# Optimization experiments

Measured on AMD Instinct MI355X. Metric: run time of the kernel, lower is better.

## Reference

```python
import jax, jax.numpy as jnp
import numpy as np

NPOINT, RADIUS, NSAMPLE = 512, 0.2, 32
EPS = 1e-5
CHANNELS = [67, 64, 64, 128]


def _fps(pts, npoint):
    # pts: [B, N, 3]; deterministic start at index 0 (torch impl uses randint)
    B, N, _ = pts.shape
    def body(carry, _):
        mind, far = carry
        c = jnp.take_along_axis(pts, far[:, None, None], axis=1)         # [B,1,3]
        mind = jnp.minimum(mind, jnp.sum((pts - c) ** 2, axis=-1))
        return (mind, jnp.argmax(mind, axis=-1).astype(jnp.int32)), far
    init = (jnp.full((B, N), 1e10, pts.dtype), jnp.zeros((B,), jnp.int32))
    _, idxs = jax.lax.scan(body, init, None, length=npoint)
    return idxs.T                                                         # [B, npoint]


def _gather(p, idx):
    # p: [B, N, C], idx: [B, ...] -> [B, ..., C]
    return jax.vmap(lambda pp, ii: pp[ii])(p, idx)


def _cbr(x, w, b, g, be, m, v):
    # Conv3d kernel [1, 4, 1]; torch padding='same' on even kernel -> (lo=1, hi=2) on t axis
    y = jax.lax.conv_general_dilated(x, w, (1, 1, 1),
                                     [(0, 0), (1, 2), (0, 0)],
                                     dimension_numbers=('NCDHW', 'OIDHW', 'NCDHW'))
    ex = lambda a: a[None, :, None, None, None]
    y = y + ex(b)
    # BatchNorm3d (eval mode with running stats)
    y = (y - ex(m)) * ex(g / jnp.sqrt(v + EPS)) + ex(be)
    return jax.nn.relu(y)


def _forward(xyz, points, params):
    B, t, _, N = xyz.shape
    S, K = NPOINT, NSAMPLE
    xf = jnp.transpose(xyz, (0, 1, 3, 2)).reshape(B * t, N, 3)            # [BT,N,3]
    pf = jnp.transpose(points, (0, 1, 3, 2)).reshape(B * t, N, -1)        # [BT,N,D]
    fidx = _fps(xf.reshape(B, t, N, 3)[:, 0], S)                          # [B,S], FPS on frame 0
    fidx_bt = jnp.broadcast_to(fidx[:, None, :], (B, t, S)).reshape(B * t, S)
    new_xyz = _gather(xf, fidx_bt)                                        # [BT,S,3]
    # squared distances via matmul form (matches square_distance)
    sq = (jnp.sum(new_xyz ** 2, -1)[:, :, None] + jnp.sum(xf ** 2, -1)[:, None, :]
          - 2.0 * jnp.einsum('bsc,bnc->bsn', new_xyz, xf))                # [BT,S,N]
    # ball query: invalid -> N, sort indices, take first K, fallback to first valid
    gidx = jnp.where(sq > RADIUS ** 2, N, jnp.arange(N, dtype=jnp.int32)[None, None, :])
    gidx = jnp.sort(gidx, axis=-1)[:, :, :K]                              # [BT,S,K]
    gidx = jnp.where(gidx == N, gidx[:, :, :1], gidx)
    gxyz = _gather(xf, gidx) - new_xyz[:, :, None, :]                     # [BT,S,K,3]
    feat = jnp.concatenate([gxyz, _gather(pf, gidx)], axis=-1)            # [BT,S,K,3+D]
    feat = feat.reshape(B, t, S, K, -1).transpose(0, 4, 2, 1, 3)          # [B,C,S,t,K]
    for p in params:
        feat = _cbr(feat, *p)
    feat = jnp.max(feat, axis=-1)                                         # [B,C',S,t]
    new_points = jnp.transpose(feat, (0, 3, 1, 2))                        # [B,t,C',S]
    new_xyz = new_xyz.reshape(B, t, S, 3).transpose(0, 1, 3, 2)           # [B,t,3,S]
    return new_xyz, new_points


def setup_inputs() -> dict:
    key = jax.random.key(0)
    ks = jax.random.split(key, 40)
    B, t, D, N = 2, 8, 64, 1024
    inp = {
        'xyz': jax.random.uniform(ks[0], (B, t, 3, N), jnp.float32),
        'points': jax.random.normal(ks[1], (B, t, D, N), jnp.float32),
    }
    j = 2
    for i in range(3):
        ci, co = CHANNELS[i], CHANNELS[i + 1]
        inp[f'w{i}'] = jax.random.normal(ks[j], (co, ci, 1, 4, 1), jnp.float32) * 0.05; j += 1
        inp[f'b{i}'] = jax.random.normal(ks[j], (co,), jnp.float32) * 0.01; j += 1
        inp[f'g{i}'] = jax.random.uniform(ks[j], (co,), jnp.float32, 0.5, 1.5); j += 1
        inp[f'be{i}'] = jax.random.normal(ks[j], (co,), jnp.float32) * 0.1; j += 1
        inp[f'm{i}'] = jax.random.normal(ks[j], (co,), jnp.float32) * 0.1; j += 1
        inp[f'v{i}'] = jax.random.uniform(ks[j], (co,), jnp.float32, 0.5, 1.5); j += 1
    return inp


def reference(xyz, points, w0, b0, g0, be0, m0, v0, w1, b1, g1, be1, m1, v1, w2, b2, g2, be2, m2, v2):
    params = [(w0, b0, g0, be0, m0, v0), (w1, b1, g1, be1, m1, v1), (w2, b2, g2, be2, m2, v2)]
    return _forward(xyz, points, params)
```

## Files before the change

kernel.cpp:

```cpp
#include <hip/hip_runtime.h>
#include <math.h>

#define NPTS 1024
#define S_   512
#define T_   8
#define K_   32
#define B_   2

typedef short bf16x8 __attribute__((ext_vector_type(8)));
typedef short short4v __attribute__((ext_vector_type(4)));
typedef float f32x4 __attribute__((ext_vector_type(4)));
typedef float vf2 __attribute__((ext_vector_type(2)));

static __device__ __forceinline__ short f2bf(float f) {
    unsigned u = __float_as_uint(f);
    unsigned r = (u + 0x7FFFu + ((u >> 16) & 1u)) >> 16;
    return (short)r;
}

template <int CTRL>
static __device__ __forceinline__ float dppmaxf(float x) {
    int mv = __builtin_amdgcn_update_dpp(0, __float_as_int(x), CTRL, 0xF, 0xF, true);
    return fmaxf(x, __int_as_float(mv));
}
static __device__ __forceinline__ unsigned wavemax_bits_f(float x) {
    x = dppmaxf<0x111>(x); x = dppmaxf<0x112>(x);
    x = dppmaxf<0x114>(x); x = dppmaxf<0x118>(x);
    x = dppmaxf<0x142>(x); x = dppmaxf<0x143>(x);
    return (unsigned)__builtin_amdgcn_readlane(__float_as_int(x), 63);
}

static __device__ __forceinline__ vf2 pk_sub(vf2 a, vf2 b) { return a - b; }
static __device__ __forceinline__ vf2 pk_fma(vf2 a, vf2 b, vf2 c) {
#if __has_builtin(__builtin_elementwise_fma)
    return __builtin_elementwise_fma(a, b, c);
#else
    vf2 r; r[0] = __fmaf_rn(a[0], b[0], c[0]); r[1] = __fmaf_rn(a[1], b[1], c[1]); return r;
#endif
}
static __device__ __forceinline__ vf2 pk_min(vf2 a, vf2 b) {
#if __has_builtin(__builtin_elementwise_min)
    return __builtin_elementwise_min(a, b);
#else
    vf2 r; r[0] = fminf(a[0], b[0]); r[1] = fminf(a[1], b[1]); return r;
#endif
}
static __device__ __forceinline__ vf2 pk_max(vf2 a, vf2 b) {
#if __has_builtin(__builtin_elementwise_max)
    return __builtin_elementwise_max(a, b);
#else
    vf2 r; r[0] = fmaxf(a[0], b[0]); r[1] = fmaxf(a[1], b[1]); return r;
#endif
}

__global__ __launch_bounds__(64) void fps_kernel(const float* __restrict__ xyz,
                                                 int* __restrict__ fidx)
{
    int b    = blockIdx.x;
    int lane = threadIdx.x;
    __shared__ float4 sc[NPTS];
    const float* bx = xyz + (size_t)b * (T_ * 3 * NPTS);
    vf2 px2[8], py2[8], pz2[8], mind2[8];
#pragma unroll
    for (int q = 0; q < 4; ++q) {
        float4 vx = ((const float4*)(bx))[lane * 4 + q];
        float4 vy = ((const float4*)(bx + NPTS))[lane * 4 + q];
        float4 vz = ((const float4*)(bx + 2 * NPTS))[lane * 4 + q];
        px2[q*2]   = (vf2){vx.x, vx.y};  px2[q*2+1] = (vf2){vx.z, vx.w};
        py2[q*2]   = (vf2){vy.x, vy.y};  py2[q*2+1] = (vf2){vy.z, vy.w};
        pz2[q*2]   = (vf2){vz.x, vz.y};  pz2[q*2+1] = (vf2){vz.z, vz.w};
        int n0 = lane * 16 + q * 4;
        sc[n0+0] = make_float4(vx.x, vy.x, vz.x, 0.f);
        sc[n0+1] = make_float4(vx.y, vy.y, vz.y, 0.f);
        sc[n0+2] = make_float4(vx.z, vy.z, vz.z, 0.f);
        sc[n0+3] = make_float4(vx.w, vy.w, vz.w, 0.f);
        mind2[q*2] = (vf2){1e10f, 1e10f}; mind2[q*2+1] = (vf2){1e10f, 1e10f};
    }
    __syncthreads();

    int far = 0;
    for (int it = 0; it < S_; ++it) {
        if (lane == 0) fidx[b * S_ + it] = far;
        float4 c = sc[far];
        vf2 c2x = (vf2){c.x, c.x}, c2y = (vf2){c.y, c.y}, c2z = (vf2){c.z, c.z};
#pragma unroll
        for (int q = 0; q < 8; ++q) {
            vf2 dx = pk_sub(px2[q], c2x);
            vf2 dy = pk_sub(py2[q], c2y);
            vf2 dz = pk_sub(pz2[q], c2z);
            vf2 d  = pk_fma(dz, dz, pk_fma(dy, dy, dx * dx));
            mind2[q] = pk_min(mind2[q], d);
        }
        vf2 t4a = pk_max(mind2[0], mind2[4]);
        vf2 t4b = pk_max(mind2[1], mind2[5]);
        vf2 t4c = pk_max(mind2[2], mind2[6]);
        vf2 t4d = pk_max(mind2[3], mind2[7]);
        vf2 t2a = pk_max(t4a, t4c);
        vf2 t2b = pk_max(t4b, t4d);
        vf2 t1  = pk_max(t2a, t2b);
        float lmax = fmaxf(t1[0], t1[1]);
        unsigned maxb = wavemax_bits_f(lmax);
        int cj[16];
#pragma unroll
        for (int j = 0; j < 16; ++j)
            cj[j] = (__float_as_uint(mind2[j >> 1][j & 1]) == maxb) ? j : 64;
        int m8[8], m4[4], m2v[2];
#pragma unroll
        for (int j = 0; j < 8; ++j) m8[j] = min(cj[j], cj[j + 8]);
#pragma unroll
        for (int j = 0; j < 4; ++j) m4[j] = min(m8[j], m8[j + 4]);
        m2v[0] = min(m4[0], m4[2]); m2v[1] = min(m4[1], m4[3]);
        int minj = min(m2v[0], m2v[1]);
        unsigned long long mk = __ballot(minj < 64);
        int l0 = __ffsll((long long)mk) - 1;
        int jw = __builtin_amdgcn_readlane(minj, l0);
        far = l0 * 16 + jw;
    }
}

__global__ __launch_bounds__(256) void transpose_points(
    const float* __restrict__ pts, short* __restrict__ ptsT)
{
    int nt = blockIdx.x;
    int bt = blockIdx.y;
    __shared__ float tile[64][65];
    int tid = threadIdx.x;
    for (int e = tid; e < 4096; e += 256) {
        int ci = e >> 6, nn = e & 63;
        tile[ci][nn] = pts[((size_t)bt * 64 + ci) * NPTS + nt * 64 + nn];
    }
    __syncthreads();
    for (int e = tid; e < 4096; e += 256) {
        int nn = e >> 6, ci = e & 63;
        ptsT[((size_t)bt * NPTS + nt * 64 + nn) * 64 + ci] = f2bf(tile[ci][nn]);
    }
}

template <int CI, int CIp, int CO, bool PERM>
__global__ __launch_bounds__(256) void prep_w(const float* __restrict__ w,
                                              short* __restrict__ wg)
{
    int e = blockIdx.x * 256 + threadIdx.x;
    if (e >= 4 * CO * CIp) return;
    int dt = e / (CO * CIp);
    int rem = e - dt * (CO * CIp);
    int co = rem / CIp;
    int ci = rem - co * CIp;
    float val = 0.0f;
    if (PERM) {
        int cref = (ci < 64) ? (ci + 3) : ((ci < 67) ? (ci - 64) : -1);
        if (cref >= 0) val = w[((size_t)co * CI + cref) * 4 + dt];
    } else {
        if (ci < CI) val = w[((size_t)co * CI + ci) * 4 + dt];
    }
    wg[e] = f2bf(val);
}

__global__ void ballquery_kernel(const float* __restrict__ xyz,
                                 const int* __restrict__ fidx,
                                 int* __restrict__ gidx,
                                 float* __restrict__ newxyz,
                                 float* __restrict__ out0)
{
    int s    = blockIdx.x;
    int bt   = blockIdx.y;
    int b    = bt >> 3;
    int lane = threadIdx.x;
    const float* bx = xyz + (size_t)bt * 3 * NPTS;
    int fid = fidx[b * S_ + s];
    float nx = bx[fid], ny = bx[NPTS + fid], nz = bx[2 * NPTS + fid];
    if (lane < 3) {
        float vv = (lane == 0) ? nx : ((lane == 1) ? ny : nz);
        out0[(bt * 3 + lane) * S_ + s]   = vv;
        newxyz[(bt * S_ + s) * 3 + lane] = vv;
    }
    float A = __fmaf_rn(nz, nz, __fmaf_rn(ny, ny, __fmul_rn(nx, nx)));
    const float R2 = (float)(0.2 * 0.2);
    int* g = gidx + (size_t)(bt * S_ + s) * K_;
    int count = 0, firstIdx = -1;
    for (int j = 0; j < 16; ++j) {
        if (count >= K_) break;
        int n = j * 64 + lane;
        float x = bx[n], y = bx[NPTS + n], z = bx[2 * NPTS + n];
        float Bn = __fmaf_rn(z, z, __fmaf_rn(y, y, __fmul_rn(x, x)));
        float C  = __fmaf_rn(nz, z, __fmaf_rn(ny, y, __fmul_rn(nx, x)));
        float sq = __fsub_rn(__fadd_rn(A, Bn), __fmul_rn(2.0f, C));
        bool valid = !(sq > R2);
        unsigned long long mb = __ballot(valid);
        if (valid) {
            int pos = count + __popcll(mb & ((1ull << lane) - 1ull));
            if (pos < K_) g[pos] = n;
        }
        if (firstIdx < 0 && mb) firstIdx = j * 64 + (__ffsll((long long)mb) - 1);
        count += __popcll(mb);
    }
    if (count < K_) {
        for (int p = count + lane; p < K_; p += 64) g[p] = firstIdx;
    }
}

template <int CI, int CIp, int NK, int CO, bool GATHER, bool POOL>
__global__ __launch_bounds__(256) void conv_mfma(
    const short* __restrict__ actIn,
    const float* __restrict__ xyz, const short* __restrict__ ptsT,
    const int* __restrict__ gidx, const float* __restrict__ newxyz,
    const short* __restrict__ wg, const float* __restrict__ bb,
    const float* __restrict__ gg, const float* __restrict__ be,
    const float* __restrict__ mm, const float* __restrict__ vv,
    short* __restrict__ actOut, float* __restrict__ outPool)
{
    __shared__ __align__(16) short xs[256 * CIp];
    int s = blockIdx.x, b = blockIdx.y;
    int co_base = blockIdx.z * 64;
    int tid = threadIdx.x;

    {
        int col = tid;
        short* xrow = &xs[col * CIp];
        if (GATHER) {
            int k = col & 31, tt = col >> 5;
            int bt = b * T_ + tt;
            int idx = gidx[((size_t)bt * S_ + s) * K_ + k];
            const short* prow = ptsT + ((size_t)bt * NPTS + idx) * 64;
#pragma unroll
            for (int c = 0; c < 8; ++c)
                ((int4*)xrow)[c] = ((const int4*)prow)[c];
            const float* nxp = &newxyz[((size_t)bt * S_ + s) * 3];
#pragma unroll
            for (int ci = 0; ci < 3; ++ci)
                xrow[64 + ci] = f2bf(xyz[(size_t)(bt * 3 + ci) * NPTS + idx] - nxp[ci]);
            for (int ci = 67; ci < CIp; ++ci) xrow[ci] = 0;
        } else {
            const short* src = actIn + (((size_t)b * S_ + s) * 256 + col) * 64;
#pragma unroll
            for (int c = 0; c < 8; ++c)
                ((int4*)xrow)[c] = ((const int4*)src)[c];
            for (int ci = 64; ci < CIp; ++ci) xrow[ci] = 0;
        }
    }
    __syncthreads();

    int lane = tid & 63;
    int wv   = tid >> 6;
    int l16  = lane & 15;
    int lq   = lane >> 4;

    f32x4 acc[16];
#pragma unroll
    for (int nb = 0; nb < 16; ++nb) acc[nb] = (f32x4){0.f, 0.f, 0.f, 0.f};

#pragma unroll
    for (int ks = 0; ks < NK; ++ks) {
        bf16x8 afr[4];
#pragma unroll
        for (int dt = 0; dt < 4; ++dt)
            afr[dt] = *(const bf16x8*)&wg[((size_t)(dt * CO + co_base + wv * 16 + l16)) * CIp + ks * 32 + lq * 8];
        bf16x8 bfr[16];
#pragma unroll
        for (int cb = 0; cb < 16; ++cb)
            bfr[cb] = *(const bf16x8*)&xs[(cb * 16 + l16) * CIp + ks * 32 + lq * 8];
#pragma unroll
        for (int dt = 0; dt < 4; ++dt) {
#pragma unroll
            for (int nb = 0; nb < 16; ++nb) {
                int cb = nb + (dt - 1) * 2;
                if (cb >= 0 && cb < 16)
                    acc[nb] = __builtin_amdgcn_mfma_f32_16x16x32_bf16(
                        afr[dt], bfr[cb], acc[nb], 0, 0, 0);
            }
        }
    }

    float sc[4], c2[4];
#pragma unroll
    for (int j = 0; j < 4; ++j) {
        int co = co_base + wv * 16 + lq * 4 + j;
        float scv = gg[co] / sqrtf(vv[co] + 1e-5f);
        sc[j] = scv;
        c2[j] = (bb[co] - mm[co]) * scv + be[co];
    }

    if (POOL) {
#pragma unroll
        for (int nbp = 0; nbp < 8; ++nbp) {
#pragma unroll
            for (int j = 0; j < 4; ++j) {
                float v0 = fmaxf(acc[2 * nbp][j] * sc[j] + c2[j], 0.0f);
                float v1 = fmaxf(acc[2 * nbp + 1][j] * sc[j] + c2[j], 0.0f);
                float v = fmaxf(v0, v1);
#pragma unroll
                for (int off = 1; off < 16; off <<= 1)
                    v = fmaxf(v, __shfl_xor(v, off));
                if (l16 == 0) {
                    int co = co_base + wv * 16 + lq * 4 + j;
                    outPool[((size_t)(b * T_ + nbp) * 128 + co) * S_ + s] = v;
                }
            }
        }
    } else {
#pragma unroll
        for (int nb = 0; nb < 16; ++nb) {
            int col = nb * 16 + l16;
            short4v pk;
#pragma unroll
            for (int j = 0; j < 4; ++j)
                pk[j] = f2bf(fmaxf(acc[nb][j] * sc[j] + c2[j], 0.0f));
            *(short4v*)&actOut[(((size_t)b * S_ + s) * 256 + col) * 64 + wv * 16 + lq * 4] = pk;
        }
    }
}

extern "C" void kernel_launch(void* const* d_in, const int* in_sizes, int n_in,
                              void* d_out, int out_size, void* d_ws, size_t ws_size,
                              hipStream_t stream)
{
    (void)in_sizes; (void)n_in; (void)out_size; (void)ws_size;
    const float* xyz    = (const float*)d_in[0];
    const float* points = (const float*)d_in[1];
    const float* w0 = (const float*)d_in[2];
    const float* b0 = (const float*)d_in[3];
    const float* g0 = (const float*)d_in[4];
    const float* be0 = (const float*)d_in[5];
    const float* m0 = (const float*)d_in[6];
    const float* v0 = (const float*)d_in[7];
    const float* w1 = (const float*)d_in[8];
    const float* b1 = (const float*)d_in[9];
    const float* g1 = (const float*)d_in[10];
    const float* be1 = (const float*)d_in[11];
    const float* m1 = (const float*)d_in[12];
    const float* v1 = (const float*)d_in[13];
    const float* w2 = (const float*)d_in[14];
    const float* b2 = (const float*)d_in[15];
    const float* g2 = (const float*)d_in[16];
    const float* be2 = (const float*)d_in[17];
    const float* m2 = (const float*)d_in[18];
    const float* v2 = (const float*)d_in[19];

    float* out = (float*)d_out;
    char* ws = (char*)d_ws;
    int*   fidx = (int*)ws;
    int*   gidx = (int*)(ws + 4096);
    float* nxyz = (float*)(ws + 4096 + 16 * 512 * 32 * 4);
    short* wg0  = (short*)(ws + (size_t)(3 * 1024 * 1024));
    short* wg1  = (short*)(ws + (size_t)(3 * 1024 * 1024) + 256 * 1024);
    short* wg2  = (short*)(ws + (size_t)(3 * 1024 * 1024) + 512 * 1024);
    short* ptsT = (short*)(ws + (size_t)(4  * 1024 * 1024));
    short* actA = (short*)(ws + (size_t)(8  * 1024 * 1024));
    short* actB = (short*)(ws + (size_t)(44 * 1024 * 1024));

    prep_w<67, 104, 64,  true ><<<(4 * 64  * 104 + 255) / 256, 256, 0, stream>>>(w0, wg0);
    prep_w<64, 72,  64,  false><<<(4 * 64  * 72  + 255) / 256, 256, 0, stream>>>(w1, wg1);
    prep_w<64, 72,  128, false><<<(4 * 128 * 72  + 255) / 256, 256, 0, stream>>>(w2, wg2);
    transpose_points<<<dim3(16, B_ * T_), 256, 0, stream>>>(points, ptsT);
    fps_kernel<<<B_, 64, 0, stream>>>(xyz, fidx);
    ballquery_kernel<<<dim3(S_, B_ * T_), 64, 0, stream>>>(xyz, fidx, gidx, nxyz, out);

    conv_mfma<67, 104, 3, 64, true, false><<<dim3(S_, B_, 1), 256, 0, stream>>>(
        nullptr, xyz, ptsT, gidx, nxyz, wg0, b0, g0, be0, m0, v0, actA, nullptr);
    conv_mfma<64, 72, 2, 64, false, false><<<dim3(S_, B_, 1), 256, 0, stream>>>(
        actA, nullptr, nullptr, nullptr, nullptr, wg1, b1, g1, be1, m1, v1, actB, nullptr);
    conv_mfma<64, 72, 2, 128, false, true><<<dim3(S_, B_, 2), 256, 0, stream>>>(
        actB, nullptr, nullptr, nullptr, nullptr, wg2, b2, g2, be2, m2, v2, nullptr,
        out + (size_t)B_ * T_ * 3 * S_);
}
```

Baseline: 345.0 us.

## Fuse ball query into conv1 and merge conv2/conv3 via LDS

Ball query now runs inside the first conv kernel, and the neighbour indices and centroids stay in shared memory. This removes a separate kernel and its gidx/newxyz round trip. The second and third conv layers are merged into one kernel, and the intermediate activation stays in LDS instead of a global buffer. Each block now computes both 64-channel halves of conv3 itself. This halves the conv3 grid and raises LDS use per block, which may lower occupancy.

```diff
diff --git a/kernel.cpp b/kernel.cpp
--- a/kernel.cpp
+++ b/kernel.cpp
@@ -156,105 +156,86 @@
     wg[e] = f2bf(val);
 }
 
-__global__ void ballquery_kernel(const float* __restrict__ xyz,
-                                 const int* __restrict__ fidx,
-                                 int* __restrict__ gidx,
-                                 float* __restrict__ newxyz,
-                                 float* __restrict__ out0)
-{
-    int s    = blockIdx.x;
-    int bt   = blockIdx.y;
-    int b    = bt >> 3;
-    int lane = threadIdx.x;
-    const float* bx = xyz + (size_t)bt * 3 * NPTS;
-    int fid = fidx[b * S_ + s];
-    float nx = bx[fid], ny = bx[NPTS + fid], nz = bx[2 * NPTS + fid];
-    if (lane < 3) {
-        float vv = (lane == 0) ? nx : ((lane == 1) ? ny : nz);
-        out0[(bt * 3 + lane) * S_ + s]   = vv;
-        newxyz[(bt * S_ + s) * 3 + lane] = vv;
-    }
-    float A = __fmaf_rn(nz, nz, __fmaf_rn(ny, ny, __fmul_rn(nx, nx)));
-    const float R2 = (float)(0.2 * 0.2);
-    int* g = gidx + (size_t)(bt * S_ + s) * K_;
-    int count = 0, firstIdx = -1;
-    for (int j = 0; j < 16; ++j) {
-        if (count >= K_) break;
-        int n = j * 64 + lane;
-        float x = bx[n], y = bx[NPTS + n], z = bx[2 * NPTS + n];
-        float Bn = __fmaf_rn(z, z, __fmaf_rn(y, y, __fmul_rn(x, x)));
-        float C  = __fmaf_rn(nz, z, __fmaf_rn(ny, y, __fmul_rn(nx, x)));
-        float sq = __fsub_rn(__fadd_rn(A, Bn), __fmul_rn(2.0f, C));
-        bool valid = !(sq > R2);
-        unsigned long long mb = __ballot(valid);
-        if (valid) {
-            int pos = count + __popcll(mb & ((1ull << lane) - 1ull));
-            if (pos < K_) g[pos] = n;
-        }
-        if (firstIdx < 0 && mb) firstIdx = j * 64 + (__ffsll((long long)mb) - 1);
-        count += __popcll(mb);
-    }
-    if (count < K_) {
-        for (int p = count + lane; p < K_; p += 64) g[p] = firstIdx;
-    }
-}
-
-template <int CI, int CIp, int NK, int CO, bool GATHER, bool POOL>
-__global__ __launch_bounds__(256) void conv_mfma(
-    const short* __restrict__ actIn,
+__global__ __launch_bounds__(256) void conv1_fused(
     const float* __restrict__ xyz, const short* __restrict__ ptsT,
-    const int* __restrict__ gidx, const float* __restrict__ newxyz,
+    const int* __restrict__ fidx,
     const short* __restrict__ wg, const float* __restrict__ bb,
     const float* __restrict__ gg, const float* __restrict__ be,
     const float* __restrict__ mm, const float* __restrict__ vv,
-    short* __restrict__ actOut, float* __restrict__ outPool)
-{
-    __shared__ __align__(16) short xs[256 * CIp];
+    short* __restrict__ actOut, float* __restrict__ out0)
+{
+    const int CIp = 104, NK = 3, CO = 64;
+    __shared__ __align__(16) short xs[256 * 104];
+    __shared__ int   gidx_l[8][K_];
+    __shared__ float nxyz_l[8][3];
     int s = blockIdx.x, b = blockIdx.y;
-    int co_base = blockIdx.z * 64;
     int tid = threadIdx.x;
+    int lane = tid & 63;
+    int wv   = tid >> 6;
+
+    int fid = fidx[b * S_ + s];
+    for (int half = 0; half < 2; ++half) {
+        int tt = wv * 2 + half;
+        int bt = b * T_ + tt;
+        const float* bx = xyz + (size_t)bt * 3 * NPTS;
+        float nx = bx[fid], ny = bx[NPTS + fid], nz = bx[2 * NPTS + fid];
+        if (lane < 3) {
+            float vvv = (lane == 0) ? nx : ((lane == 1) ? ny : nz);
+            out0[(bt * 3 + lane) * S_ + s] = vvv;
+            nxyz_l[tt][lane] = vvv;
+        }
+        float A = __fmaf_rn(nz, nz, __fmaf_rn(ny, ny, __fmul_rn(nx, nx)));
+        const float R2 = (float)(0.2 * 0.2);
+        int count = 0, firstIdx = -1;
+        for (int j = 0; j < 16; ++j) {
+            if (count >= K_) break;
+            int n = j * 64 + lane;
+            float x = bx[n], y = bx[NPTS + n], z = bx[2 * NPTS + n];
+            float Bn = __fmaf_rn(z, z, __fmaf_rn(y, y, __fmul_rn(x, x)));
+            float C  = __fmaf_rn(nz, z, __fmaf_rn(ny, y, __fmul_rn(nx, x)));
+            float sq = __fsub_rn(__fadd_rn(A, Bn), __fmul_rn(2.0f, C));
+            bool valid = !(sq > R2);
+            unsigned long long mb = __ballot(valid);
+            if (valid) {
+                int pos = count + __popcll(mb & ((1ull << lane) - 1ull));
+                if (pos < K_) gidx_l[tt][pos] = n;
+            }
+            if (firstIdx < 0 && mb) firstIdx = j * 64 + (__ffsll((long long)mb) - 1);
+            count += __popcll(mb);
+        }
+        if (count < K_) {
+            for (int p = count + lane; p < K_; p += 64) gidx_l[tt][p] = firstIdx;
+        }
+    }
+    __syncthreads();
 
     {
         int col = tid;
+        int k = col & 31, tt = col >> 5;
+        int bt = b * T_ + tt;
         short* xrow = &xs[col * CIp];
-        if (GATHER) {
-            int k = col & 31, tt = col >> 5;
-            int bt = b * T_ + tt;
-            int idx = gidx[((size_t)bt * S_ + s) * K_ + k];
-            const short* prow = ptsT + ((size_t)bt * NPTS + idx) * 64;
-#pragma unroll
-            for (int c = 0; c < 8; ++c)
-                ((int4*)xrow)[c] = ((const int4*)prow)[c];
-            const float* nxp = &newxyz[((size_t)bt * S_ + s) * 3];
-#pragma unroll
-            for (int ci = 0; ci < 3; ++ci)
-                xrow[64 + ci] = f2bf(xyz[(size_t)(bt * 3 + ci) * NPTS + idx] - nxp[ci]);
-            for (int ci = 67; ci < CIp; ++ci) xrow[ci] = 0;
-        } else {
-            const short* src = actIn + (((size_t)b * S_ + s) * 256 + col) * 64;
-#pragma unroll
-            for (int c = 0; c < 8; ++c)
-                ((int4*)xrow)[c] = ((const int4*)src)[c];
-            for (int ci = 64; ci < CIp; ++ci) xrow[ci] = 0;
-        }
-    }
-    __syncthreads();
-
-    int lane = tid & 63;
-    int wv   = tid >> 6;
-    int l16  = lane & 15;
-    int lq   = lane >> 4;
-
+        int idx = gidx_l[tt][k];
+        const short* prow = ptsT + ((size_t)bt * NPTS + idx) * 64;
+#pragma unroll
+        for (int c = 0; c < 8; ++c)
+            ((int4*)xrow)[c] = ((const int4*)prow)[c];
+#pragma unroll
+        for (int ci = 0; ci < 3; ++ci)
+            xrow[64 + ci] = f2bf(xyz[(size_t)(bt * 3 + ci) * NPTS + idx] - nxyz_l[tt][ci]);
+        for (int ci = 67; ci < CIp; ++ci) xrow[ci] = 0;
+    }
+    __syncthreads();
+
+    int l16 = lane & 15, lq = lane >> 4;
     f32x4 acc[16];
 #pragma unroll
     for (int nb = 0; nb < 16; ++nb) acc[nb] = (f32x4){0.f, 0.f, 0.f, 0.f};
-
 #pragma unroll
     for (int ks = 0; ks < NK; ++ks) {
         bf16x8 afr[4];
 #pragma unroll
         for (int dt = 0; dt < 4; ++dt)
-            afr[dt] = *(const bf16x8*)&wg[((size_t)(dt * CO + co_base + wv * 16 + l16)) * CIp + ks * 32 + lq * 8];
+            afr[dt] = *(const bf16x8*)&wg[((size_t)(dt * CO + wv * 16 + l16)) * CIp + ks * 32 + lq * 8];
         bf16x8 bfr[16];
 #pragma unroll
         for (int cb = 0; cb < 16; ++cb)
@@ -270,17 +251,136 @@
             }
         }
     }
-
     float sc[4], c2[4];
 #pragma unroll
     for (int j = 0; j < 4; ++j) {
-        int co = co_base + wv * 16 + lq * 4 + j;
+        int co = wv * 16 + lq * 4 + j;
         float scv = gg[co] / sqrtf(vv[co] + 1e-5f);
         sc[j] = scv;
         c2[j] = (bb[co] - mm[co]) * scv + be[co];
     }
-
-    if (POOL) {
+#pragma unroll
+    for (int nb = 0; nb < 16; ++nb) {
+        int col = nb * 16 + l16;
+        short4v pk;
+#pragma unroll
+        for (int j = 0; j < 4; ++j)
+            pk[j] = f2bf(fmaxf(acc[nb][j] * sc[j] + c2[j], 0.0f));
+        *(short4v*)&actOut[(((size_t)b * S_ + s) * 256 + col) * 64 + wv * 16 + lq * 4] = pk;
+    }
+}
+
+__global__ __launch_bounds__(256) void conv23_fused(
+    const short* __restrict__ actIn,
+    const short* __restrict__ wg1, const float* __restrict__ bb1,
+    const float* __restrict__ gg1, const float* __restrict__ be1,
+    const float* __restrict__ mm1, const float* __restrict__ vv1,
+    const short* __restrict__ wg2, const float* __restrict__ bb2,
+    const float* __restrict__ gg2, const float* __restrict__ be2,
+    const float* __restrict__ mm2, const float* __restrict__ vv2,
+    float* __restrict__ outPool)
+{
+    const int CIp = 72, NK = 2;
+    __shared__ __align__(16) short xs2[256 * 72];
+    __shared__ __align__(16) short xs3[256 * 72];
+    int s = blockIdx.x, b = blockIdx.y;
+    int tid = threadIdx.x;
+    int lane = tid & 63;
+    int wv   = tid >> 6;
+    int l16  = lane & 15;
+    int lq   = lane >> 4;
+
+    {
+        int col = tid;
+        short* xrow = &xs2[col * CIp];
+        const short* src = actIn + (((size_t)b * S_ + s) * 256 + col) * 64;
+#pragma unroll
+        for (int c = 0; c < 8; ++c)
+            ((int4*)xrow)[c] = ((const int4*)src)[c];
+        short* xrow3 = &xs3[col * CIp];
+        for (int ci = 64; ci < CIp; ++ci) { xrow[ci] = 0; xrow3[ci] = 0; }
+    }
+    __syncthreads();
+
+    {
+        f32x4 acc[16];
+#pragma unroll
+        for (int nb = 0; nb < 16; ++nb) acc[nb] = (f32x4){0.f, 0.f, 0.f, 0.f};
+#pragma unroll
+        for (int ks = 0; ks < NK; ++ks) {
+            bf16x8 afr[4];
+#pragma unroll
+            for (int dt = 0; dt < 4; ++dt)
+                afr[dt] = *(const bf16x8*)&wg1[((size_t)(dt * 64 + wv * 16 + l16)) * CIp + ks * 32 + lq * 8];
+            bf16x8 bfr[16];
+#pragma unroll
+            for (int cb = 0; cb < 16; ++cb)
+                bfr[cb] = *(const bf16x8*)&xs2[(cb * 16 + l16) * CIp + ks * 32 + lq * 8];
+#pragma unroll
+            for (int dt = 0; dt < 4; ++dt) {
+#pragma unroll
+                for (int nb = 0; nb < 16; ++nb) {
+                    int cb = nb + (dt - 1) * 2;
+                    if (cb >= 0 && cb < 16)
+                        acc[nb] = __builtin_amdgcn_mfma_f32_16x16x32_bf16(
+                            afr[dt], bfr[cb], acc[nb], 0, 0, 0);
+                }
+            }
+        }
+        float sc[4], c2[4];
+#pragma unroll
+        for (int j = 0; j < 4; ++j) {
+            int co = wv * 16 + lq * 4 + j;
+            float scv = gg1[co] / sqrtf(vv1[co] + 1e-5f);
+            sc[j] = scv;
+            c2[j] = (bb1[co] - mm1[co]) * scv + be1[co];
+        }
+#pragma unroll
+        for (int nb = 0; nb < 16; ++nb) {
+            int col = nb * 16 + l16;
+            short4v pk;
+#pragma unroll
+            for (int j = 0; j < 4; ++j)
+                pk[j] = f2bf(fmaxf(acc[nb][j] * sc[j] + c2[j], 0.0f));
+            *(short4v*)&xs3[col * CIp + wv * 16 + lq * 4] = pk;
+        }
+    }
+    __syncthreads();
+
+#pragma unroll
+    for (int st = 0; st < 2; ++st) {
+        f32x4 acc[16];
+#pragma unroll
+        for (int nb = 0; nb < 16; ++nb) acc[nb] = (f32x4){0.f, 0.f, 0.f, 0.f};
+#pragma unroll
+        for (int ks = 0; ks < NK; ++ks) {
+            bf16x8 afr[4];
+#pragma unroll
+            for (int dt = 0; dt < 4; ++dt)
+                afr[dt] = *(const bf16x8*)&wg2[((size_t)(dt * 128 + st * 64 + wv * 16 + l16)) * CIp + ks * 32 + lq * 8];
+            bf16x8 bfr[16];
+#pragma unroll
+            for (int cb = 0; cb < 16; ++cb)
+                bfr[cb] = *(const bf16x8*)&xs3[(cb * 16 + l16) * CIp + ks * 32 + lq * 8];
+#pragma unroll
+            for (int dt = 0; dt < 4; ++dt) {
+#pragma unroll
+                for (int nb = 0; nb < 16; ++nb) {
+                    int cb = nb + (dt - 1) * 2;
+                    if (cb >= 0 && cb < 16)
+                        acc[nb] = __builtin_amdgcn_mfma_f32_16x16x32_bf16(
+                            afr[dt], bfr[cb], acc[nb], 0, 0, 0);
+                }
+            }
+        }
+        float sc[4], c2[4];
+#pragma unroll
+        for (int j = 0; j < 4; ++j) {
+            int co = st * 64 + wv * 16 + lq * 4 + j;
+            float scv = gg2[co] / sqrtf(vv2[co] + 1e-5f);
+            sc[j] = scv;
+            c2[j] = (bb2[co] - mm2[co]) * scv + be2[co];
+        }
 #pragma unroll
         for (int nbp = 0; nbp < 8; ++nbp) {
 #pragma unroll
@@ -292,20 +392,10 @@
                 for (int off = 1; off < 16; off <<= 1)
                     v = fmaxf(v, __shfl_xor(v, off));
                 if (l16 == 0) {
-                    int co = co_base + wv * 16 + lq * 4 + j;
+                    int co = st * 64 + wv * 16 + lq * 4 + j;
                     outPool[((size_t)(b * T_ + nbp) * 128 + co) * S_ + s] = v;
                 }
             }
-        }
-    } else {
-#pragma unroll
-        for (int nb = 0; nb < 16; ++nb) {
-            int col = nb * 16 + l16;
-            short4v pk;
-#pragma unroll
-            for (int j = 0; j < 4; ++j)
-                pk[j] = f2bf(fmaxf(acc[nb][j] * sc[j] + c2[j], 0.0f));
-            *(short4v*)&actOut[(((size_t)b * S_ + s) * 256 + col) * 64 + wv * 16 + lq * 4] = pk;
         }
     }
 }
@@ -339,27 +429,21 @@
     float* out = (float*)d_out;
     char* ws = (char*)d_ws;
     int*   fidx = (int*)ws;
-    int*   gidx = (int*)(ws + 4096);
-    float* nxyz = (float*)(ws + 4096 + 16 * 512 * 32 * 4);
     short* wg0  = (short*)(ws + (size_t)(3 * 1024 * 1024));
     short* wg1  = (short*)(ws + (size_t)(3 * 1024 * 1024) + 256 * 1024);
     short* wg2  = (short*)(ws + (size_t)(3 * 1024 * 1024) + 512 * 1024);
     short* ptsT = (short*)(ws + (size_t)(4  * 1024 * 1024));
     short* actA = (short*)(ws + (size_t)(8  * 1024 * 1024));
-    short* actB = (short*)(ws + (size_t)(44 * 1024 * 1024));
 
     prep_w<67, 104, 64,  true ><<<(4 * 64  * 104 + 255) / 256, 256, 0, stream>>>(w0, wg0);
     prep_w<64, 72,  64,  false><<<(4 * 64  * 72  + 255) / 256, 256, 0, stream>>>(w1, wg1);
     prep_w<64, 72,  128, false><<<(4 * 128 * 72  + 255) / 256, 256, 0, stream>>>(w2, wg2);
     transpose_points<<<dim3(16, B_ * T_), 256, 0, stream>>>(points, ptsT);
     fps_kernel<<<B_, 64, 0, stream>>>(xyz, fidx);
-    ballquery_kernel<<<dim3(S_, B_ * T_), 64, 0, stream>>>(xyz, fidx, gidx, nxyz, out);
-
-    conv_mfma<67, 104, 3, 64, true, false><<<dim3(S_, B_, 1), 256, 0, stream>>>(
-        nullptr, xyz, ptsT, gidx, nxyz, wg0, b0, g0, be0, m0, v0, actA, nullptr);
-    conv_mfma<64, 72, 2, 64, false, false><<<dim3(S_, B_, 1), 256, 0, stream>>>(
-        actA, nullptr, nullptr, nullptr, nullptr, wg1, b1, g1, be1, m1, v1, actB, nullptr);
-    conv_mfma<64, 72, 2, 128, false, true><<<dim3(S_, B_, 2), 256, 0, stream>>>(
-        actB, nullptr, nullptr, nullptr, nullptr, wg2, b2, g2, be2, m2, v2, nullptr,
+
+    conv1_fused<<<dim3(S_, B_), 256, 0, stream>>>(
+        xyz, ptsT, fidx, wg0, b0, g0, be0, m0, v0, actA, out);
+    conv23_fused<<<dim3(S_, B_), 256, 0, stream>>>(
+        actA, wg1, b1, g1, be1, m1, v1, wg2, b2, g2, be2, m2, v2,
         out + (size_t)B_ * T_ * 3 * S_);
 }
```

Result: slower. 354.3 us (+2.7%).
